# Kernel optimization log

Measured on AMD Instinct MI355X. Metric: run time of the kernel, lower is better.

## Reference

```python
import jax, jax.numpy as jnp
import numpy as np

B, H, W, K = 4, 512, 512, 8
BKG_DEPTH = 100.0  # sentinel depth for empty pixels, as in the torch module


def setup_inputs() -> dict:
    key = jax.random.key(0)
    k1, k2, k3 = jax.random.split(key, 3)
    pixel_colors = jax.random.uniform(k1, (B, H, W, K, 4), dtype=jnp.float32)
    zbuf = jax.random.normal(k2, (B, H, W, K), dtype=jnp.float32)  # <0 => invalid fragment
    pixel_labels = jax.random.randint(k3, (B, H, W, K), 0, K, dtype=jnp.int32)
    background_color = jnp.ones((3,), jnp.float32)
    return {
        "pixel_colors": pixel_colors,
        "zbuf": zbuf,
        "pixel_labels": pixel_labels,
        "background_color": background_color,
    }


def _composite(pixel_colors, zbuf, labels_f, background_color):
    """Back-to-front alpha-over compositing scan across the K layer axis."""
    Bq, Hq, Wq, Kd, _ = pixel_colors.shape
    # layer axis to front, reversed so scan runs k = K-1 .. 0 (back to front)
    cols = jnp.moveaxis(pixel_colors, 3, 0)[::-1]  # [K,B,H,W,4]
    deps = jnp.moveaxis(zbuf, 3, 0)[::-1]          # [K,B,H,W]
    labs = jnp.moveaxis(labels_f, 3, 0)[::-1]      # [K,B,H,W]

    rgb0 = jnp.broadcast_to(background_color.astype(pixel_colors.dtype), (Bq, Hq, Wq, 3)) + 0.0
    a0 = jnp.zeros((Bq, Hq, Wq), pixel_colors.dtype)
    d0 = jnp.full((Bq, Hq, Wq), BKG_DEPTH, pixel_colors.dtype)
    l0 = jnp.full((Bq, Hq, Wq), float(Kd), pixel_colors.dtype)

    def step(carry, x):
        rgb, a, d, lab = carry
        c, z, l = x
        alpha = c[..., 3]
        rgb = c[..., :3] * alpha[..., None] + rgb * (1.0 - alpha[..., None])
        a = jnp.maximum(alpha, a)
        d = jnp.where(z > 0, z * alpha + d * (1.0 - alpha), d)
        lab = jnp.where(jnp.isfinite(l), jnp.where(alpha > 0.5, l, lab), lab)
        return (rgb, a, d, lab), None

    (rgb, a, d, lab), _ = jax.lax.scan(step, (rgb0, a0, d0, l0), (cols, deps, labs))
    img = jnp.concatenate([rgb, a[..., None]], axis=-1)  # [B,H,W,4]
    return img, d, lab


def _human_images(pixel_colors, labels_int, background_color):
    """For each label n in [0,K): gather the first (front-most) fragment with that label."""
    Bq, Hq, Wq, Kd, C = pixel_colors.shape
    N = Kd
    hit = labels_int[..., None] == jnp.arange(N, dtype=labels_int.dtype)  # [B,H,W,K,N]
    hit = jnp.concatenate([hit, jnp.ones((Bq, Hq, Wq, 1, N), bool)], axis=3)  # void layer always hits
    first = jnp.argmax(hit, axis=3)  # [B,H,W,N], first k where label matches, else K
    pcv = jnp.concatenate(
        [pixel_colors, jnp.zeros((Bq, Hq, Wq, 1, C), pixel_colors.dtype)], axis=3
    )  # [B,H,W,K+1,4]
    gathered = jnp.take_along_axis(pcv, first[..., None], axis=3)  # [B,H,W,N,4]
    alpha = gathered[..., 3:4]
    rgb = gathered[..., :3] * alpha + background_color * (1.0 - alpha)
    return jnp.concatenate([rgb, alpha], axis=-1)  # [B,H,W,N,4]


def reference(pixel_colors, zbuf, pixel_labels, background_color):
    Kd = pixel_colors.shape[3]
    # labels as float with NaN marking invalid fragments (zbuf < 0), as in torch forward
    labels_f = jnp.where(zbuf < 0, jnp.nan, pixel_labels.astype(pixel_colors.dtype))
    composite_image, composite_depth, lab = _composite(pixel_colors, zbuf, labels_f, background_color)
    # labels as ints with -1 marking invalid, as in raster_each_labeled_human
    labels_int = jnp.where(zbuf < 0, -1, pixel_labels.astype(jnp.int32))
    human_images = _human_images(pixel_colors, labels_int, background_color)
    lab = jnp.where(lab > Kd - 0.5, -1.0, lab)
    composite_label = jnp.round(lab).astype(jnp.int32)
    return composite_image, composite_depth, composite_label, human_images
```

## Files before the change

kernel.cpp:

```cpp
#include <hip/hip_runtime.h>


#define BKG_DEPTH 100.0f
#define KD 8

__global__ __launch_bounds__(256) void alpha_comp_kernel(
    const float4* __restrict__ pc,
    const float4* __restrict__ zb,
    const int4*   __restrict__ lb,
    const float*  __restrict__ bg,
    float* __restrict__ out,
    int P)
{
    __shared__ float4 lds[256 * 9];

    const int t = threadIdx.x;
    const int pix = blockIdx.x * 256 + t;
    const size_t fragBase = (size_t)blockIdx.x * 2048;

    const float bg0 = bg[0], bg1 = bg[1], bg2 = bg[2];

#pragma unroll
    for (int i = 0; i < 8; ++i) {
        const int f = i * 256 + t;
        const float4 v = pc[fragBase + f];
        lds[(f >> 3) * 9 + (f & 7)] = v;
    }
    __syncthreads();

    float4 c[KD];
#pragma unroll
    for (int k = 0; k < KD; ++k) c[k] = lds[t * 9 + k];

    const float4 z0 = zb[(size_t)pix * 2 + 0];
    const float4 z1 = zb[(size_t)pix * 2 + 1];
    const float z[KD] = {z0.x, z0.y, z0.z, z0.w, z1.x, z1.y, z1.z, z1.w};

    const int4 l0 = lb[(size_t)pix * 2 + 0];
    const int4 l1 = lb[(size_t)pix * 2 + 1];
    const int lbl[KD] = {l0.x, l0.y, l0.z, l0.w, l1.x, l1.y, l1.z, l1.w};

    float r = bg0, g = bg1, b = bg2;
    float a = 0.0f, d = BKG_DEPTH, lab = (float)KD;
#pragma unroll
    for (int k = KD - 1; k >= 0; --k) {
        const float alpha = c[k].w;
        const float ia = 1.0f - alpha;
        r = c[k].x * alpha + r * ia;
        g = c[k].y * alpha + g * ia;
        b = c[k].z * alpha + b * ia;
        a = fmaxf(alpha, a);
        if (z[k] > 0.0f) d = z[k] * alpha + d * ia;
        if (!(z[k] < 0.0f) && alpha > 0.5f) lab = (float)lbl[k];
    }
    const float labv = (lab > (float)KD - 0.5f) ? -1.0f : lab;

    float4 hv[KD];
#pragma unroll
    for (int n = 0; n < KD; ++n) {
        float4 gat = make_float4(0.0f, 0.0f, 0.0f, 0.0f);
#pragma unroll
        for (int k = KD - 1; k >= 0; --k) {
            if (!(z[k] < 0.0f) && lbl[k] == n) gat = c[k];
        }
        const float alpha = gat.w;
        const float ia = 1.0f - alpha;
        hv[n] = make_float4(gat.x * alpha + bg0 * ia,
                            gat.y * alpha + bg1 * ia,
                            gat.z * alpha + bg2 * ia,
                            alpha);
    }

    ((float4*)out)[pix] = make_float4(r, g, b, a);
    out[(size_t)4 * P + pix] = d;
    out[(size_t)5 * P + pix] = labv;

#pragma unroll
    for (int n = 0; n < KD; ++n) lds[t * 9 + n] = hv[n];
    __syncthreads();

    float4* outH = (float4*)(out + (size_t)6 * P);
#pragma unroll
    for (int i = 0; i < 8; ++i) {
        const int f = i * 256 + t;
        outH[fragBase + f] = lds[(f >> 3) * 9 + (f & 7)];
    }
}

extern "C" void kernel_launch(void* const* d_in, const int* in_sizes, int n_in,
                              void* d_out, int out_size, void* d_ws, size_t ws_size,
                              hipStream_t stream) {
    const float4* pc = (const float4*)d_in[0];
    const float4* zb = (const float4*)d_in[1];
    const int4*   lb = (const int4*)d_in[2];
    const float*  bg = (const float*)d_in[3];
    float* out = (float*)d_out;

    const int P = in_sizes[1] / KD;
    const int block = 256;
    const int grid = P / block;
    alpha_comp_kernel<<<grid, block, 0, stream>>>(pc, zb, lb, bg, out, P);
}
```

Measured before the change: 303.2 us.

## Drop LDS staging, process 4 pixels per thread with register prefetch and nontemporal stores

Removes the shared-memory transpose for both loads and stores. Each thread now reads its pixel's 8 float4 fragments directly and writes its 8 human-image float4s directly, using nontemporal stores. Each thread handles 4 pixels strided across the image and prefetches the next pixel's inputs while computing the current one, so the grid is a quarter the size. The trade-off is per-thread strided 128-byte accesses, which coalesce less well than the old LDS-staged pattern, plus higher register pressure from double-buffering a pixel's data.

```diff
diff --git a/kernel.cpp b/kernel.cpp
--- a/kernel.cpp
+++ b/kernel.cpp
@@ -3,6 +3,79 @@
 
 #define BKG_DEPTH 100.0f
 #define KD 8
+#define PPT 4
+
+typedef float float4n __attribute__((ext_vector_type(4)));
+
+struct Px {
+    float4 c[KD];
+    float  z[KD];
+    int    l[KD];
+};
+
+__device__ __forceinline__ void load_px(const float4* __restrict__ pc,
+                                        const float4* __restrict__ zb,
+                                        const int4*   __restrict__ lb,
+                                        int pix, Px& p)
+{
+#pragma unroll
+    for (int k = 0; k < KD; ++k) p.c[k] = pc[(size_t)pix * KD + k];
+    const float4 z0 = zb[(size_t)pix * 2 + 0];
+    const float4 z1 = zb[(size_t)pix * 2 + 1];
+    p.z[0]=z0.x; p.z[1]=z0.y; p.z[2]=z0.z; p.z[3]=z0.w;
+    p.z[4]=z1.x; p.z[5]=z1.y; p.z[6]=z1.z; p.z[7]=z1.w;
+    const int4 l0 = lb[(size_t)pix * 2 + 0];
+    const int4 l1 = lb[(size_t)pix * 2 + 1];
+    p.l[0]=l0.x; p.l[1]=l0.y; p.l[2]=l0.z; p.l[3]=l0.w;
+    p.l[4]=l1.x; p.l[5]=l1.y; p.l[6]=l1.z; p.l[7]=l1.w;
+}
+
+__device__ __forceinline__ void nt_store4(float* addr, float x, float y, float z, float w)
+{
+    float4n v; v.x = x; v.y = y; v.z = z; v.w = w;
+    __builtin_nontemporal_store(v, (float4n*)addr);
+}
+
+__device__ __forceinline__ void process_store(const Px& p, int pix, int P,
+                                              float bg0, float bg1, float bg2,
+                                              float* __restrict__ out)
+{
+    float r = bg0, g = bg1, b = bg2;
+    float a = 0.0f, d = BKG_DEPTH, lab = (float)KD;
+#pragma unroll
+    for (int k = KD - 1; k >= 0; --k) {
+        const float alpha = p.c[k].w;
+        const float ia = 1.0f - alpha;
+        r = p.c[k].x * alpha + r * ia;
+        g = p.c[k].y * alpha + g * ia;
+        b = p.c[k].z * alpha + b * ia;
+        a = fmaxf(alpha, a);
+        if (p.z[k] > 0.0f) d = p.z[k] * alpha + d * ia;
+        if (!(p.z[k] < 0.0f) && alpha > 0.5f) lab = (float)p.l[k];
+    }
+    const float labv = (lab > (float)KD - 0.5f) ? -1.0f : lab;
+
+    nt_store4(out + (size_t)pix * 4, r, g, b, a);
+    __builtin_nontemporal_store(d,    out + (size_t)4 * P + pix);
+    __builtin_nontemporal_store(labv, out + (size_t)5 * P + pix);
+
+    float* outH = out + (size_t)6 * P + (size_t)pix * KD * 4;
+#pragma unroll
+    for (int n = 0; n < KD; ++n) {
+        float4 gat = make_float4(0.0f, 0.0f, 0.0f, 0.0f);
+#pragma unroll
+        for (int k = KD - 1; k >= 0; --k) {
+            if (!(p.z[k] < 0.0f) && p.l[k] == n) gat = p.c[k];
+        }
+        const float alpha = gat.w;
+        const float ia = 1.0f - alpha;
+        nt_store4(outH + n * 4,
+                  gat.x * alpha + bg0 * ia,
+                  gat.y * alpha + bg1 * ia,
+                  gat.z * alpha + bg2 * ia,
+                  alpha);
+    }
+}
 
 __global__ __launch_bounds__(256) void alpha_comp_kernel(
     const float4* __restrict__ pc,
@@ -12,78 +85,19 @@
     float* __restrict__ out,
     int P)
 {
-    __shared__ float4 lds[256 * 9];
-
-    const int t = threadIdx.x;
-    const int pix = blockIdx.x * 256 + t;
-    const size_t fragBase = (size_t)blockIdx.x * 2048;
+    const int tid = blockIdx.x * blockDim.x + threadIdx.x;
+    const int stride = P / PPT;
+    if (tid >= stride) return;
 
     const float bg0 = bg[0], bg1 = bg[1], bg2 = bg[2];
 
+    Px cur, nxt;
+    load_px(pc, zb, lb, tid, cur);
 #pragma unroll
-    for (int i = 0; i < 8; ++i) {
-        const int f = i * 256 + t;
-        const float4 v = pc[fragBase + f];
-        lds[(f >> 3) * 9 + (f & 7)] = v;
-    }
-    __syncthreads();
-
-    float4 c[KD];
-#pragma unroll
-    for (int k = 0; k < KD; ++k) c[k] = lds[t * 9 + k];
-
-    const float4 z0 = zb[(size_t)pix * 2 + 0];
-    const float4 z1 = zb[(size_t)pix * 2 + 1];
-    const float z[KD] = {z0.x, z0.y, z0.z, z0.w, z1.x, z1.y, z1.z, z1.w};
-
-    const int4 l0 = lb[(size_t)pix * 2 + 0];
-    const int4 l1 = lb[(size_t)pix * 2 + 1];
-    const int lbl[KD] = {l0.x, l0.y, l0.z, l0.w, l1.x, l1.y, l1.z, l1.w};
-
-    float r = bg0, g = bg1, b = bg2;
-    float a = 0.0f, d = BKG_DEPTH, lab = (float)KD;
-#pragma unroll
-    for (int k = KD - 1; k >= 0; --k) {
-        const float alpha = c[k].w;
-        const float ia = 1.0f - alpha;
-        r = c[k].x * alpha + r * ia;
-        g = c[k].y * alpha + g * ia;
-        b = c[k].z * alpha + b * ia;
-        a = fmaxf(alpha, a);
-        if (z[k] > 0.0f) d = z[k] * alpha + d * ia;
-        if (!(z[k] < 0.0f) && alpha > 0.5f) lab = (float)lbl[k];
-    }
-    const float labv = (lab > (float)KD - 0.5f) ? -1.0f : lab;
-
-    float4 hv[KD];
-#pragma unroll
-    for (int n = 0; n < KD; ++n) {
-        float4 gat = make_float4(0.0f, 0.0f, 0.0f, 0.0f);
-#pragma unroll
-        for (int k = KD - 1; k >= 0; --k) {
-            if (!(z[k] < 0.0f) && lbl[k] == n) gat = c[k];
-        }
-        const float alpha = gat.w;
-        const float ia = 1.0f - alpha;
-        hv[n] = make_float4(gat.x * alpha + bg0 * ia,
-                            gat.y * alpha + bg1 * ia,
-                            gat.z * alpha + bg2 * ia,
-                            alpha);
-    }
-
-    ((float4*)out)[pix] = make_float4(r, g, b, a);
-    out[(size_t)4 * P + pix] = d;
-    out[(size_t)5 * P + pix] = labv;
-
-#pragma unroll
-    for (int n = 0; n < KD; ++n) lds[t * 9 + n] = hv[n];
-    __syncthreads();
-
-    float4* outH = (float4*)(out + (size_t)6 * P);
-#pragma unroll
-    for (int i = 0; i < 8; ++i) {
-        const int f = i * 256 + t;
-        outH[fragBase + f] = lds[(f >> 3) * 9 + (f & 7)];
+    for (int r = 0; r < PPT; ++r) {
+        if (r + 1 < PPT) load_px(pc, zb, lb, tid + (r + 1) * stride, nxt);
+        process_store(cur, tid + r * stride, P, bg0, bg1, bg2, out);
+        if (r + 1 < PPT) cur = nxt;
     }
 }
 
@@ -97,7 +111,8 @@
     float* out = (float*)d_out;
 
     const int P = in_sizes[1] / KD;
+    const int threads = P / PPT;
     const int block = 256;
-    const int grid = P / block;
+    const int grid = threads / block;
     alpha_comp_kernel<<<grid, block, 0, stream>>>(pc, zb, lb, bg, out, P);
 }
```

After: 613.7 us. 102% more time.
